# Kernel tuning notes

Hardware: AMD Instinct MI355X
Metric: run time of the kernel (lower is better)

The kernel has to match this reference:

```python
import jax, jax.numpy as jnp
import numpy as np

B, S, L, H, D, FF, V = 2, 1024, 12, 12, 768, 3072, 50265
DH = D // H
W1 = 256                      # one-sided window (attention_window=512)
MOTIF = (31 + 96 + 80) * 2    # 414
MAXPOS = 4098
EPS = 1e-5
NEG = jnp.float32(-1e9)


def _ln(x, s, b):
    m = jnp.mean(x, -1, keepdims=True)
    v = jnp.mean(jnp.square(x - m), -1, keepdims=True)
    return (x - m) * jax.lax.rsqrt(v + EPS) * s + b


def setup_inputs() -> dict:
    key = jax.random.key(0)
    ks = iter(jax.random.split(key, 48))
    n = lambda *sh: jax.random.normal(next(ks), sh, jnp.float32) * 0.02
    return {
        "input_ids": jax.random.randint(next(ks), (B, S), 0, V),
        "attention_mask": jnp.ones((B, S), jnp.int32),
        "motif_dist": jax.random.uniform(next(ks), (B, MOTIF), dtype=jnp.float32),
        "emb_word": n(V, D), "emb_pos": n(MAXPOS, D), "emb_type": n(1, D),
        "emb_ln_s": jnp.ones((D,)), "emb_ln_b": jnp.zeros((D,)),
        "Wq": n(L, D, D), "bq": jnp.zeros((L, D)),
        "Wk": n(L, D, D), "bk": jnp.zeros((L, D)),
        "Wv": n(L, D, D), "bv": jnp.zeros((L, D)),
        "Wqg": n(L, D, D), "bqg": jnp.zeros((L, D)),
        "Wkg": n(L, D, D), "bkg": jnp.zeros((L, D)),
        "Wvg": n(L, D, D), "bvg": jnp.zeros((L, D)),
        "Wo": n(L, D, D), "bo": jnp.zeros((L, D)),
        "ln1_s": jnp.ones((L, D)), "ln1_b": jnp.zeros((L, D)),
        "Wi": n(L, D, FF), "bi": jnp.zeros((L, FF)),
        "Wo2": n(L, FF, D), "bo2": jnp.zeros((L, D)),
        "ln2_s": jnp.ones((L, D)), "ln2_b": jnp.zeros((L, D)),
        "head_Wd": n(D + MOTIF, D), "head_bd": jnp.zeros((D,)),
        "head_Wp": n(D, 2), "head_bp": jnp.zeros((2,)),
    }


def reference(input_ids, attention_mask, motif_dist, emb_word, emb_pos, emb_type,
              emb_ln_s, emb_ln_b, Wq, bq, Wk, bk, Wv, bv, Wqg, bqg, Wkg, bkg,
              Wvg, bvg, Wo, bo, ln1_s, ln1_b, Wi, bi, Wo2, bo2, ln2_s, ln2_b,
              head_Wd, head_bd, head_Wp, head_bp):
    Bn, Sn = input_ids.shape
    scale = 1.0 / np.sqrt(DH)
    # RoBERTa-style embeddings: positions start at padding_idx+1 = 2
    pos_ids = jnp.arange(Sn) + 2
    x = emb_word[input_ids] + emb_pos[pos_ids][None] + emb_type[0][None, None]
    x = _ln(x, emb_ln_s, emb_ln_b)

    key_valid = attention_mask.astype(bool)[:, None, None, :]      # [B,1,1,S]
    idx = jnp.arange(Sn)
    is_global = idx == 0                                           # default: CLS-only global
    band = jnp.abs(idx[:, None] - idx[None, :]) <= W1
    # local query attends to its sliding window plus all global keys
    local_allowed = (band | is_global[None, :])[None, None] & key_valid

    def heads(t, s):
        return t.reshape(Bn, s, H, DH).transpose(0, 2, 1, 3)       # [B,H,s,DH]

    for l in range(L):
        q = heads(x @ Wq[l] + bq[l], Sn) * scale
        k = heads(x @ Wk[l] + bk[l], Sn)
        v = heads(x @ Wv[l] + bv[l], Sn)
        scores = jnp.einsum('bhid,bhjd->bhij', q, k)
        probs = jax.nn.softmax(jnp.where(local_allowed, scores, NEG), -1)
        out = jnp.einsum('bhij,bhjd->bhid', probs, v)              # [B,H,S,DH]
        # global (CLS) query: full attention using the *_global projections
        qg = heads(x[:, :1] @ Wqg[l] + bqg[l], 1) * scale          # [B,H,1,DH]
        kg = heads(x @ Wkg[l] + bkg[l], Sn)
        vg = heads(x @ Wvg[l] + bvg[l], Sn)
        sg = jnp.einsum('bhid,bhjd->bhij', qg, kg)                 # [B,H,1,S]
        pg = jax.nn.softmax(jnp.where(key_valid, sg, NEG), -1)
        og = jnp.einsum('bhij,bhjd->bhid', pg, vg)                 # [B,H,1,DH]
        out = jnp.concatenate([og, out[:, :, 1:]], axis=2)
        out = out.transpose(0, 2, 1, 3).reshape(Bn, Sn, D)
        x = _ln(x + out @ Wo[l] + bo[l], ln1_s[l], ln1_b[l])
        h = jax.nn.gelu(x @ Wi[l] + bi[l], approximate=False)
        x = _ln(x + h @ Wo2[l] + bo2[l], ln2_s[l], ln2_b[l])

    # classification head: CLS hidden state concat motif distribution
    hcat = jnp.concatenate([x[:, 0, :], motif_dist], axis=-1)
    return jnp.tanh(hcat @ head_Wd + head_bd) @ head_Wp + head_bp
```

## Files before the change

kernel.cpp:

```cpp
#include <hip/hip_runtime.h>
#include <math.h>

typedef unsigned short u16;
typedef __attribute__((ext_vector_type(8))) short short8;
typedef __attribute__((ext_vector_type(4))) float f32x4;

#define BB 2
#define SS 1024
#define LL 12
#define HH 12
#define DD 768
#define FFF 3072
#define MOTIF 414
#define HCAT (DD + MOTIF)
#define W1 256
#define NEGV -1e9f
#define EPS 1e-5f
#define SCALE 0.125f
#define LD5 3840

__device__ __forceinline__ float bf2f(u16 u) {
    union { unsigned i; float f; } x; x.i = ((unsigned)u) << 16; return x.f;
}
__device__ __forceinline__ u16 f2bf(float f) {
    union { float f; unsigned i; } x; x.f = f;
    unsigned r = x.i + 0x7fffu + ((x.i >> 16) & 1u);
    return (u16)(r >> 16);
}

__device__ __forceinline__ void gld16(const u16* g, u16* l) {
    __builtin_amdgcn_global_load_lds((const __attribute__((address_space(1))) void*)g,
                                     (__attribute__((address_space(3))) void*)l, 16, 0, 0);
}

__device__ __forceinline__ float block_reduce_sum(float v, float* red) {
    int t = threadIdx.x;
    red[t] = v; __syncthreads();
    #pragma unroll
    for (int s = 128; s > 0; s >>= 1) {
        if (t < s) red[t] += red[t + s];
        __syncthreads();
    }
    float r = red[0]; __syncthreads();
    return r;
}

__global__ __launch_bounds__(256) void embed_ln_kernel(
    const int* __restrict__ ids, const float* __restrict__ ew,
    const float* __restrict__ ep, const float* __restrict__ et,
    const float* __restrict__ gs, const float* __restrict__ gb,
    float* __restrict__ X, u16* __restrict__ Xb) {
    __shared__ float red[256];
    int row = blockIdx.x;
    int s = row % SS;
    int id = ids[row];
    int t = threadIdx.x;
    float v[3];
    float sum = 0.f;
    #pragma unroll
    for (int i = 0; i < 3; ++i) {
        int d = t + 256 * i;
        float x = ew[(size_t)id * DD + d] + ep[(size_t)(s + 2) * DD + d] + et[d];
        v[i] = x; sum += x;
    }
    sum = block_reduce_sum(sum, red);
    float m = sum * (1.f / DD);
    float sq = 0.f;
    #pragma unroll
    for (int i = 0; i < 3; ++i) { float c = v[i] - m; sq += c * c; }
    sq = block_reduce_sum(sq, red);
    float inv = rsqrtf(sq * (1.f / DD) + EPS);
    #pragma unroll
    for (int i = 0; i < 3; ++i) {
        int d = t + 256 * i;
        float o = (v[i] - m) * inv * gs[d] + gb[d];
        X[(size_t)row * DD + d] = o;
        Xb[(size_t)row * DD + d] = f2bf(o);
    }
}

__global__ __launch_bounds__(256) void add_ln_kernel(
    float* __restrict__ X, u16* __restrict__ Xb,
    const float* __restrict__ T1, const float* __restrict__ T2, int useT2,
    const float* __restrict__ gs, const float* __restrict__ gb) {
    __shared__ float red[256];
    int row = blockIdx.x;
    int t = threadIdx.x;
    float v[3];
    float sum = 0.f;
    #pragma unroll
    for (int i = 0; i < 3; ++i) {
        int d = t + 256 * i;
        size_t idx = (size_t)row * DD + d;
        float x = X[idx] + T1[idx] + (useT2 ? T2[idx] : 0.f);
        v[i] = x; sum += x;
    }
    sum = block_reduce_sum(sum, red);
    float m = sum * (1.f / DD);
    float sq = 0.f;
    #pragma unroll
    for (int i = 0; i < 3; ++i) { float c = v[i] - m; sq += c * c; }
    sq = block_reduce_sum(sq, red);
    float inv = rsqrtf(sq * (1.f / DD) + EPS);
    #pragma unroll
    for (int i = 0; i < 3; ++i) {
        int d = t + 256 * i;
        float o = (v[i] - m) * inv * gs[d] + gb[d];
        X[(size_t)row * DD + d] = o;
        Xb[(size_t)row * DD + d] = f2bf(o);
    }
}

__global__ __launch_bounds__(256) void conv_all_kernel(
    const float* __restrict__ w0, const float* __restrict__ w1,
    const float* __restrict__ w2, const float* __restrict__ w3,
    const float* __restrict__ w4, const float* __restrict__ w5,
    const float* __restrict__ wi, const float* __restrict__ wo2,
    u16* __restrict__ Wt6, u16* __restrict__ Wti, u16* __restrict__ Wto2) {
    __shared__ float Tt[32][33];
    int tid = blockIdx.x;
    const float* W; u16* Wt; int Nd, Kd, n0, k0;
    if (tid < 3456) {
        int z = tid / 576, rem = tid % 576;
        W = (z == 0) ? w0 : (z == 1) ? w1 : (z == 2) ? w2 : (z == 3) ? w3 : (z == 4) ? w4 : w5;
        Wt = Wt6 + (size_t)z * DD * DD;
        Nd = DD; Kd = DD; n0 = (rem % 24) * 32; k0 = (rem / 24) * 32;
    } else if (tid < 5760) {
        int i = tid - 3456;
        W = wi; Wt = Wti; Nd = FFF; Kd = DD; n0 = (i % 96) * 32; k0 = (i / 96) * 32;
    } else {
        int i = tid - 5760;
        W = wo2; Wt = Wto2; Nd = DD; Kd = FFF; n0 = (i % 24) * 32; k0 = (i / 24) * 32;
    }
    int t = threadIdx.x;
    int r = t >> 3, c = (t & 7) * 4;
    float4 v = *(const float4*)(W + (size_t)(k0 + r) * Nd + n0 + c);
    Tt[r][c] = v.x; Tt[r][c + 1] = v.y; Tt[r][c + 2] = v.z; Tt[r][c + 3] = v.w;
    __syncthreads();
    int n = t >> 3, k4 = (t & 7) * 4;
    unsigned lo = (unsigned)f2bf(Tt[k4][n])     | ((unsigned)f2bf(Tt[k4 + 1][n]) << 16);
    unsigned hi = (unsigned)f2bf(Tt[k4 + 2][n]) | ((unsigned)f2bf(Tt[k4 + 3][n]) << 16);
    uint2 wv; wv.x = lo; wv.y = hi;
    *(uint2*)&Wt[(size_t)(n0 + n) * Kd + k0 + k4] = wv;
}

__global__ __launch_bounds__(256) void bcat_kernel(
    const float* __restrict__ bq, const float* __restrict__ bk,
    const float* __restrict__ bv, const float* __restrict__ bkg,
    const float* __restrict__ bvg, float* __restrict__ bcat) {
    int tid = blockIdx.x * 256 + threadIdx.x;
    if (tid >= LL * LD5) return;
    int l = tid / LD5, r = tid % LD5, z = r / DD, j = r % DD;
    const float* src = (z == 0) ? bq : (z == 1) ? bk : (z == 2) ? bv : (z == 3) ? bkg : bvg;
    bcat[tid] = src[l * DD + j];
}

template <int ACT, int OBF>
__global__ __launch_bounds__(256) void gemm_bf16(
    const u16* __restrict__ A, const u16* __restrict__ Bt,
    const float* __restrict__ bias, void* __restrict__ C0, void* __restrict__ C1,
    int M, int N, int K, int Ksplit) {
    __shared__ __align__(16) u16 As[128 * 32];
    __shared__ __align__(16) u16 Bs[128 * 32];
    int z = blockIdx.z;
    int kbeg = z * Ksplit;
    int kend = kbeg + Ksplit; if (kend > K) kend = K;
    void* Cout = z ? C1 : C0;
    int t = threadIdx.x, lane = t & 63, wv = t >> 6;
    int bm = blockIdx.y * 128, bn = blockIdx.x * 128;
    int wm = wv >> 1, wn = wv & 1;
    int h = lane >> 4, q15 = lane & 15;
    f32x4 acc[4][4];
    #pragma unroll
    for (int i = 0; i < 4; ++i)
        #pragma unroll
        for (int j = 0; j < 4; ++j) { acc[i][j][0] = 0.f; acc[i][j][1] = 0.f; acc[i][j][2] = 0.f; acc[i][j][3] = 0.f; }

    for (int k0 = kbeg; k0 < kend; k0 += 32) {
        #pragma unroll
        for (int op = 0; op < 2; ++op) {
            int rc = wv * 32 + op * 16;
            int r = rc + (lane >> 2), s = lane & 3;
            gld16(A  + (size_t)(bm + r) * K + k0 + ((s ^ (r & 3)) * 8), &As[rc * 32]);
            gld16(Bt + (size_t)(bn + r) * K + k0 + ((s ^ (r & 3)) * 8), &Bs[rc * 32]);
        }
        __syncthreads();
        short8 af[4], bfr[4];
        #pragma unroll
        for (int mf = 0; mf < 4; ++mf) {
            int row = wm * 64 + mf * 16 + q15;
            af[mf] = *(const short8*)&As[row * 32 + ((h ^ (row & 3)) * 8)];
        }
        #pragma unroll
        for (int nf = 0; nf < 4; ++nf) {
            int row = wn * 64 + nf * 16 + q15;
            bfr[nf] = *(const short8*)&Bs[row * 32 + ((h ^ (row & 3)) * 8)];
        }
        #pragma unroll
        for (int mf = 0; mf < 4; ++mf)
            #pragma unroll
            for (int nf = 0; nf < 4; ++nf)
                acc[mf][nf] = __builtin_amdgcn_mfma_f32_16x16x32_bf16(af[mf], bfr[nf], acc[mf][nf], 0, 0, 0);
        __syncthreads();
    }
    float* Cf = (float*)Cout;
    u16*   Cb = (u16*)Cout;
    #pragma unroll
    for (int mf = 0; mf < 4; ++mf) {
        int mbase = bm + wm * 64 + mf * 16 + h * 4;
        #pragma unroll
        for (int nf = 0; nf < 4; ++nf) {
            int n = bn + wn * 64 + nf * 16 + q15;
            float bv = 0.f;
            if (z == 0) bv = bias[n];
            #pragma unroll
            for (int rg = 0; rg < 4; ++rg) {
                float val = acc[mf][nf][rg] + bv;
                if (ACT == 1) val = 0.5f * val * (1.f + erff(val * 0.70710678118654752f));
                if (OBF) Cb[(size_t)(mbase + rg) * N + n] = f2bf(val);
                else     Cf[(size_t)(mbase + rg) * N + n] = val;
            }
        }
    }
}

__global__ __launch_bounds__(256) void attn_local_mfma(
    const u16* __restrict__ QKV, const int* __restrict__ mask,
    u16* __restrict__ AO) {
    __shared__ __align__(16) u16 Qs[64 * 64];
    __shared__ __align__(16) u16 Ks[64 * 64];
    __shared__ __align__(16) u16 Vst[64 * 64];
    __shared__ __align__(16) u16 Pld[4][16 * 64];
    __shared__ float msk[64];
    int bid = blockIdx.x;
    int qt = bid & 15;
    int hh = (bid >> 4) % HH;
    int b  = bid / (16 * HH);
    int t = threadIdx.x, lane = t & 63, wv = t >> 6;
    int h = lane >> 4, q15 = lane & 15;
    int i0 = qt * 64;

    #pragma unroll
    for (int op = 0; op < 2; ++op) {
        int r = wv * 16 + op * 8 + (lane >> 3), s = lane & 7;
        gld16(QKV + (size_t)(b * SS + i0 + r) * LD5 + hh * 64 + ((s ^ (r & 7)) * 8),
              &Qs[(wv * 16 + op * 8) * 64]);
    }
    __syncthreads();
    short8 bq[2];
    {
        int qrow = wv * 16 + q15;
        #pragma unroll
        for (int ks = 0; ks < 2; ++ks)
            bq[ks] = *(const short8*)&Qs[qrow * 64 + (((ks * 4 + h) ^ (qrow & 7)) * 8)];
    }

    float mrun = -3e38f, lrun = 0.f;
    f32x4 o[4];
    #pragma unroll
    for (int nf = 0; nf < 4; ++nf) { o[nf][0] = 0.f; o[nf][1] = 0.f; o[nf][2] = 0.f; o[nf][3] = 0.f; }

    int jlo = i0 - W1; if (jlo < 0) jlo = 0;
    int jend = i0 + 64 + W1; if (jend > SS) jend = SS;
    int hasCLS = (jlo > 0) ? 1 : 0;
    int nt = hasCLS + (jend - jlo) / 64;
    int iq = i0 + wv * 16 + q15;

    for (int tt = 0; tt < nt; ++tt) {
        int base = (hasCLS && tt == 0) ? 0 : jlo + (tt - hasCLS) * 64;
        if (tt > 0) __syncthreads();
        #pragma unroll
        for (int op = 0; op < 2; ++op) {
            int r = wv * 16 + op * 8 + (lane >> 3), s = lane & 7;
            gld16(QKV + (size_t)(b * SS + base + r) * LD5 + 768 + hh * 64 + ((s ^ (r & 7)) * 8),
                  &Ks[(wv * 16 + op * 8) * 64]);
        }
        {
            int k2 = t & 31, dsec = t >> 5;
            const u16* vp = QKV + (size_t)(b * SS + base + 2 * k2) * LD5 + 1536 + hh * 64 + dsec * 8;
            union { uint4 v; u16 e[8]; } r0, r1;
            r0.v = *(const uint4*)vp;
            r1.v = *(const uint4*)(vp + LD5);
            int slot = k2 >> 2;
            #pragma unroll
            for (int j = 0; j < 8; ++j) {
                int d = dsec * 8 + j;
                unsigned val = (unsigned)r0.e[j] | ((unsigned)r1.e[j] << 16);
                *(unsigned*)&Vst[d * 64 + ((slot ^ (d & 7)) * 8) + ((2 * k2) & 7)] = val;
            }
        }
        if (t < 64) msk[t] = (float)mask[b * SS + base + t];
        __syncthreads();

        f32x4 sacc[4];
        #pragma unroll
        for (int kf = 0; kf < 4; ++kf) { sacc[kf][0] = 0.f; sacc[kf][1] = 0.f; sacc[kf][2] = 0.f; sacc[kf][3] = 0.f; }
        #pragma unroll
        for (int ks = 0; ks < 2; ++ks) {
            #pragma unroll
            for (int kf = 0; kf < 4; ++kf) {
                int krow = kf * 16 + q15;
                short8 afr = *(const short8*)&Ks[krow * 64 + (((ks * 4 + h) ^ (krow & 7)) * 8)];
                sacc[kf] = __builtin_amdgcn_mfma_f32_16x16x32_bf16(afr, bq[ks], sacc[kf], 0, 0, 0);
            }
        }
        float pv[4][4];
        float tmax = -3e38f;
        #pragma unroll
        for (int kf = 0; kf < 4; ++kf) {
            #pragma unroll
            for (int rg = 0; rg < 4; ++rg) {
                int kl = kf * 16 + h * 4 + rg;
                int key = base + kl;
                int dj = iq - key; int adj = dj < 0 ? -dj : dj;
                bool valid = ((adj <= W1) || (key == 0)) && (msk[kl] != 0.f);
                float s = valid ? sacc[kf][rg] * SCALE : NEGV;
                pv[kf][rg] = s;
                tmax = fmaxf(tmax, s);
            }
        }
        tmax = fmaxf(tmax, __shfl_xor(tmax, 16));
        tmax = fmaxf(tmax, __shfl_xor(tmax, 32));
        float mnew = fmaxf(mrun, tmax);
        float fac = __expf(mrun - mnew);
        mrun = mnew;
        float psum = 0.f;
        #pragma unroll
        for (int kf = 0; kf < 4; ++kf)
            #pragma unroll
            for (int rg = 0; rg < 4; ++rg) {
                float p = __expf(pv[kf][rg] - mnew);
                pv[kf][rg] = p; psum += p;
            }
        psum += __shfl_xor(psum, 16);
        psum += __shfl_xor(psum, 32);
        lrun = lrun * fac + psum;
        #pragma unroll
        for (int kf = 0; kf < 4; ++kf) {
            unsigned lo = (unsigned)f2bf(pv[kf][0]) | ((unsigned)f2bf(pv[kf][1]) << 16);
            unsigned hi = (unsigned)f2bf(pv[kf][2]) | ((unsigned)f2bf(pv[kf][3]) << 16);
            int slot = 2 * kf + (h >> 1);
            uint2 w; w.x = lo; w.y = hi;
            *(uint2*)&Pld[wv][q15 * 64 + ((slot ^ (q15 & 7)) * 8) + 4 * (h & 1)] = w;
        }
        float fo0 = __shfl(fac, (h * 4 + 0) | (lane & 48));
        float fo1 = __shfl(fac, (h * 4 + 1) | (lane & 48));
        float fo2 = __shfl(fac, (h * 4 + 2) | (lane & 48));
        float fo3 = __shfl(fac, (h * 4 + 3) | (lane & 48));
        #pragma unroll
        for (int nf = 0; nf < 4; ++nf) {
            o[nf][0] *= fo0; o[nf][1] *= fo1; o[nf][2] *= fo2; o[nf][3] *= fo3;
        }
        asm volatile("s_waitcnt lgkmcnt(0)" ::: "memory");
        #pragma unroll
        for (int ks = 0; ks < 2; ++ks) {
            short8 ap = *(const short8*)&Pld[wv][q15 * 64 + (((ks * 4 + h) ^ (q15 & 7)) * 8)];
            #pragma unroll
            for (int nf = 0; nf < 4; ++nf) {
                int d = nf * 16 + q15;
                short8 bvf = *(const short8*)&Vst[d * 64 + (((ks * 4 + h) ^ (d & 7)) * 8)];
                o[nf] = __builtin_amdgcn_mfma_f32_16x16x32_bf16(ap, bvf, o[nf], 0, 0, 0);
            }
        }
    }
    float linv = 1.f / lrun;
    float g0 = __shfl(linv, (h * 4 + 0) | (lane & 48));
    float g1 = __shfl(linv, (h * 4 + 1) | (lane & 48));
    float g2 = __shfl(linv, (h * 4 + 2) | (lane & 48));
    float g3 = __shfl(linv, (h * 4 + 3) | (lane & 48));
    size_t rb = (size_t)(b * SS + i0 + wv * 16 + h * 4);
    #pragma unroll
    for (int nf = 0; nf < 4; ++nf) {
        int d = hh * 64 + nf * 16 + q15;
        AO[(rb + 0) * DD + d] = f2bf(o[nf][0] * g0);
        AO[(rb + 1) * DD + d] = f2bf(o[nf][1] * g1);
        AO[(rb + 2) * DD + d] = f2bf(o[nf][2] * g2);
        AO[(rb + 3) * DD + d] = f2bf(o[nf][3] * g3);
    }
}

__global__ __launch_bounds__(512) void attn_global_kernel(
    const float* __restrict__ Xf, const float* __restrict__ Wqg,
    const float* __restrict__ bqg, const u16* __restrict__ QKV,
    const int* __restrict__ mask, u16* __restrict__ AO) {
    __shared__ float x0[DD];
    __shared__ float qv[64];
    __shared__ float sc[SS];
    __shared__ float red[512];
    __shared__ float part[8][64];
    int b = blockIdx.x / HH, hh = blockIdx.x % HH;
    int t = threadIdx.x;
    for (int i = t; i < DD; i += 512) x0[i] = Xf[(size_t)b * SS * DD + i];
    __syncthreads();
    {
        int d = t & 63, p = t >> 6;
        float acc = 0.f;
        int k0 = p * 96;
        #pragma unroll 8
        for (int k = k0; k < k0 + 96; ++k)
            acc += x0[k] * Wqg[(size_t)k * DD + hh * 64 + d];
        part[p][d] = acc;
    }
    __syncthreads();
    if (t < 64) {
        float s = bqg[hh * 64 + t];
        #pragma unroll
        for (int p = 0; p < 8; ++p) s += part[p][t];
        qv[t] = s * SCALE;
    }
    __syncthreads();
    for (int j = t; j < SS; j += 512) {
        const u16* kp = QKV + (size_t)(b * SS + j) * LD5 + 2304 + hh * 64;
        float acc = 0.f;
        #pragma unroll
        for (int d0 = 0; d0 < 64; d0 += 8) {
            union { uint4 v; u16 e[8]; } u;
            u.v = *(const uint4*)(kp + d0);
            #pragma unroll
            for (int j2 = 0; j2 < 8; ++j2) acc += qv[d0 + j2] * bf2f(u.e[j2]);
        }
        sc[j] = mask[b * SS + j] ? acc : NEGV;
    }
    __syncthreads();
    float mx = fmaxf(sc[t], sc[t + 512]);
    red[t] = mx; __syncthreads();
    #pragma unroll
    for (int s = 256; s > 0; s >>= 1) {
        if (t < s) red[t] = fmaxf(red[t], red[t + s]);
        __syncthreads();
    }
    mx = red[0]; __syncthreads();
    float e0 = __expf(sc[t] - mx), e1 = __expf(sc[t + 512] - mx);
    sc[t] = e0; sc[t + 512] = e1;
    red[t] = e0 + e1; __syncthreads();
    #pragma unroll
    for (int s = 256; s > 0; s >>= 1) {
        if (t < s) red[t] += red[t + s];
        __syncthreads();
    }
    float lsum = red[0]; __syncthreads();
    int g = t >> 6, d = t & 63;
    float acc = 0.f;
    for (int j = g; j < SS; j += 8)
        acc += sc[j] * bf2f(QKV[(size_t)(b * SS + j) * LD5 + 3072 + hh * 64 + d]);
    part[g][d] = acc;
    __syncthreads();
    if (g == 0) {
        float ov = 0.f;
        #pragma unroll
        for (int p = 0; p < 8; ++p) ov += part[p][d];
        AO[(size_t)(b * SS) * DD + hh * 64 + d] = f2bf(ov / lsum);
    }
}

__global__ __launch_bounds__(256) void head1_kernel(
    const float* __restrict__ X, const float* __restrict__ motif,
    const float* __restrict__ Wd, float* __restrict__ hpart) {
    __shared__ float hc[HCAT];
    __shared__ float part[4][64];
    int jb = blockIdx.x, kp = blockIdx.y, b = blockIdx.z;
    int t = threadIdx.x;
    for (int i = t; i < DD; i += 256) hc[i] = X[(size_t)b * SS * DD + i];
    for (int i = t; i < MOTIF; i += 256) hc[DD + i] = motif[(size_t)b * MOTIF + i];
    __syncthreads();
    int j = jb * 64 + (t & 63);
    int sub = t >> 6;
    int k0 = kp * 148 + sub * 37;
    int k1 = k0 + 37; if (k1 > HCAT) k1 = HCAT;
    float acc = 0.f;
    for (int k = k0; k < k1; ++k) acc += hc[k] * Wd[(size_t)k * DD + j];
    part[sub][t & 63] = acc;
    __syncthreads();
    if (sub == 0) {
        int x = t & 63;
        hpart[((size_t)b * 8 + kp) * DD + j] = part[0][x] + part[1][x] + part[2][x] + part[3][x];
    }
}

__global__ __launch_bounds__(256) void head2_kernel(
    const float* __restrict__ hpart, const float* __restrict__ bd,
    const float* __restrict__ Wp, const float* __restrict__ bp,
    float* __restrict__ out) {
    __shared__ float dvs[DD];
    __shared__ float red[256];
    int b = blockIdx.x;
    int t = threadIdx.x;
    for (int j = t; j < DD; j += 256) {
        float s = bd[j];
        #pragma unroll
        for (int kp = 0; kp < 8; ++kp) s += hpart[((size_t)b * 8 + kp) * DD + j];
        dvs[j] = tanhf(s);
    }
    __syncthreads();
    float a0 = 0.f, a1 = 0.f;
    for (int k = t; k < DD; k += 256) {
        a0 += dvs[k] * Wp[k * 2 + 0];
        a1 += dvs[k] * Wp[k * 2 + 1];
    }
    a0 = block_reduce_sum(a0, red);
    a1 = block_reduce_sum(a1, red);
    if (t == 0) {
        out[b * 2 + 0] = a0 + bp[0];
        out[b * 2 + 1] = a1 + bp[1];
    }
}

extern "C" void kernel_launch(void* const* d_in, const int* in_sizes, int n_in,
                              void* d_out, int out_size, void* d_ws, size_t ws_size,
                              hipStream_t stream) {
    const int*   input_ids = (const int*)d_in[0];
    const int*   attn_mask = (const int*)d_in[1];
    const float* motif     = (const float*)d_in[2];
    const float* emb_word  = (const float*)d_in[3];
    const float* emb_pos   = (const float*)d_in[4];
    const float* emb_type  = (const float*)d_in[5];
    const float* emb_ln_s  = (const float*)d_in[6];
    const float* emb_ln_b  = (const float*)d_in[7];
    const float* Wq  = (const float*)d_in[8];
    const float* bq  = (const float*)d_in[9];
    const float* Wk  = (const float*)d_in[10];
    const float* bk  = (const float*)d_in[11];
    const float* Wv  = (const float*)d_in[12];
    const float* bv  = (const float*)d_in[13];
    const float* Wqg = (const float*)d_in[14];
    const float* bqg = (const float*)d_in[15];
    const float* Wkg = (const float*)d_in[16];
    const float* bkg = (const float*)d_in[17];
    const float* Wvg = (const float*)d_in[18];
    const float* bvg = (const float*)d_in[19];
    const float* Wo  = (const float*)d_in[20];
    const float* bo  = (const float*)d_in[21];
    const float* ln1_s = (const float*)d_in[22];
    const float* ln1_b = (const float*)d_in[23];
    const float* Wi  = (const float*)d_in[24];
    const float* bi  = (const float*)d_in[25];
    const float* Wo2 = (const float*)d_in[26];
    const float* bo2 = (const float*)d_in[27];
    const float* ln2_s = (const float*)d_in[28];
    const float* ln2_b = (const float*)d_in[29];
    const float* head_Wd = (const float*)d_in[30];
    const float* head_bd = (const float*)d_in[31];
    const float* head_Wp = (const float*)d_in[32];
    const float* head_bp = (const float*)d_in[33];

    float* out = (float*)d_out;
    char* base = (char*)d_ws;

    float* Xf   = (float*)(base + 0);
    u16*   Xb   = (u16*)  (base + 6291456);
    u16*   QKVb = (u16*)  (base + 9437184);
    u16*   AOb  = (u16*)  (base + 25165824);
    float* T1f  = (float*)(base + 28311552);

    const size_t NEED_BIG = 57643008;
    bool big = ws_size >= NEED_BIG;
    float* T2f = big ? (float*)(base + 34603008) : T1f;
    size_t wbase = big ? 40894464 : 34603008;
    u16*   Wt6   = (u16*)  (base + wbase);
    u16*   Wti   = (u16*)  (base + wbase + 7077888);
    u16*   Wto2  = (u16*)  (base + wbase + 11796480);
    float* bcat  = (float*)(base + wbase + 16515072);
    float* hpart = (float*)(base + wbase + 16699392);
    u16*   Hb    = QKVb;

    const int nrow = BB * SS;
    const int useT2 = big ? 1 : 0;

    embed_ln_kernel<<<nrow, 256, 0, stream>>>(input_ids, emb_word, emb_pos, emb_type,
                                              emb_ln_s, emb_ln_b, Xf, Xb);
    bcat_kernel<<<(LL * LD5 + 255) / 256, 256, 0, stream>>>(bq, bk, bv, bkg, bvg, bcat);

    dim3 g5(30, 16, 1);
    dim3 gO(6, 16, big ? 2 : 1);
    dim3 gFF1(24, 16, 1);
    dim3 gFF2(6, 16, big ? 2 : 1);

    for (int l = 0; l < LL; ++l) {
        size_t oDD = (size_t)l * DD * DD;
        conv_all_kernel<<<8064, 256, 0, stream>>>(
            Wq + oDD, Wk + oDD, Wv + oDD, Wkg + oDD, Wvg + oDD, Wo + oDD,
            Wi + (size_t)l * DD * FFF, Wo2 + (size_t)l * FFF * DD,
            Wt6, Wti, Wto2);

        gemm_bf16<0, 1><<<g5, 256, 0, stream>>>(Xb, Wt6, bcat + l * LD5, QKVb, QKVb,
                                                nrow, LD5, DD, DD);

        attn_local_mfma<<<BB * HH * 16, 256, 0, stream>>>(QKVb, attn_mask, AOb);
        attn_global_kernel<<<BB * HH, 512, 0, stream>>>(Xf, Wqg + oDD, bqg + l * DD,
                                                        QKVb, attn_mask, AOb);

        gemm_bf16<0, 0><<<gO, 256, 0, stream>>>(AOb, Wt6 + 5 * (size_t)DD * DD, bo + l * DD,
                                                T1f, T2f, nrow, DD, DD, big ? 384 : 768);
        add_ln_kernel<<<nrow, 256, 0, stream>>>(Xf, Xb, T1f, T2f, useT2,
                                                ln1_s + l * DD, ln1_b + l * DD);

        gemm_bf16<1, 1><<<gFF1, 256, 0, stream>>>(Xb, Wti, bi + l * FFF, Hb, Hb,
                                                  nrow, FFF, DD, DD);
        gemm_bf16<0, 0><<<gFF2, 256, 0, stream>>>(Hb, Wto2, bo2 + l * DD,
                                                  T1f, T2f, nrow, DD, FFF, big ? 1536 : 3072);
        add_ln_kernel<<<nrow, 256, 0, stream>>>(Xf, Xb, T1f, T2f, useT2,
                                                ln2_s + l * DD, ln2_b + l * DD);
    }

    head1_kernel<<<dim3(12, 8, BB), 256, 0, stream>>>(Xf, motif, head_Wd, hpart);
    head2_kernel<<<BB, 256, 0, stream>>>(hpart, head_Wp ? head_bd : head_bd, head_Wp, head_bp, out);
}
```

Baseline: 2.707 ms.

## Batch all-layer weight conversion into one launch and fuse local/global attention

```diff
diff --git a/kernel.cpp b/kernel.cpp
--- a/kernel.cpp
+++ b/kernel.cpp
@@ -18,6 +18,7 @@
 #define EPS 1e-5f
 #define SCALE 0.125f
 #define LD5 3840
+#define WL_ELE 8257536
 
 __device__ __forceinline__ float bf2f(u16 u) {
     union { unsigned i; float f; } x; x.i = ((unsigned)u) << 16; return x.f;
@@ -111,26 +112,34 @@
     }
 }
 
+template <int LAYERED>
 __global__ __launch_bounds__(256) void conv_all_kernel(
-    const float* __restrict__ w0, const float* __restrict__ w1,
-    const float* __restrict__ w2, const float* __restrict__ w3,
-    const float* __restrict__ w4, const float* __restrict__ w5,
-    const float* __restrict__ wi, const float* __restrict__ wo2,
-    u16* __restrict__ Wt6, u16* __restrict__ Wti, u16* __restrict__ Wto2) {
+    const float* __restrict__ Wqp, const float* __restrict__ Wkp,
+    const float* __restrict__ Wvp, const float* __restrict__ Wkgp,
+    const float* __restrict__ Wvgp, const float* __restrict__ Wop,
+    const float* __restrict__ Wip, const float* __restrict__ Wo2p,
+    u16* __restrict__ WtBase) {
     __shared__ float Tt[32][33];
+    int l = LAYERED ? blockIdx.y : 0;
+    size_t oDD = (size_t)l * DD * DD;
+    size_t oFF = (size_t)l * DD * FFF;
+    u16* Wt6  = WtBase + (size_t)l * WL_ELE;
+    u16* Wti  = Wt6 + 6 * DD * DD;
+    u16* Wto2 = Wti + FFF * DD;
     int tid = blockIdx.x;
     const float* W; u16* Wt; int Nd, Kd, n0, k0;
     if (tid < 3456) {
         int z = tid / 576, rem = tid % 576;
-        W = (z == 0) ? w0 : (z == 1) ? w1 : (z == 2) ? w2 : (z == 3) ? w3 : (z == 4) ? w4 : w5;
+        const float* w6[6] = {Wqp + oDD, Wkp + oDD, Wvp + oDD, Wkgp + oDD, Wvgp + oDD, Wop + oDD};
+        W = w6[z];
         Wt = Wt6 + (size_t)z * DD * DD;
         Nd = DD; Kd = DD; n0 = (rem % 24) * 32; k0 = (rem / 24) * 32;
     } else if (tid < 5760) {
         int i = tid - 3456;
-        W = wi; Wt = Wti; Nd = FFF; Kd = DD; n0 = (i % 96) * 32; k0 = (i / 96) * 32;
+        W = Wip + oFF; Wt = Wti; Nd = FFF; Kd = DD; n0 = (i % 96) * 32; k0 = (i / 96) * 32;
     } else {
         int i = tid - 5760;
-        W = wo2; Wt = Wto2; Nd = DD; Kd = FFF; n0 = (i % 24) * 32; k0 = (i / 24) * 32;
+        W = Wo2p + oFF; Wt = Wto2; Nd = DD; Kd = FFF; n0 = (i % 24) * 32; k0 = (i / 24) * 32;
     }
     int t = threadIdx.x;
     int r = t >> 3, c = (t & 7) * 4;
@@ -224,19 +233,99 @@
     }
 }
 
-__global__ __launch_bounds__(256) void attn_local_mfma(
+struct LocalS {
+    u16 Qs[64 * 64]; u16 Ks[64 * 64]; u16 Vst[64 * 64];
+    u16 Pld[4][16 * 64]; float msk[64];
+};
+struct GlobS {
+    float x0[DD]; float qv[64]; float sc[SS]; float red[256]; float part[4][64];
+};
+union __align__(16) AttnSU { LocalS l; GlobS g; };
+
+__global__ __launch_bounds__(256) void attn_fused(
     const u16* __restrict__ QKV, const int* __restrict__ mask,
-    u16* __restrict__ AO) {
-    __shared__ __align__(16) u16 Qs[64 * 64];
-    __shared__ __align__(16) u16 Ks[64 * 64];
-    __shared__ __align__(16) u16 Vst[64 * 64];
-    __shared__ __align__(16) u16 Pld[4][16 * 64];
-    __shared__ float msk[64];
+    const float* __restrict__ Xf, const float* __restrict__ Wqg,
+    const float* __restrict__ bqg, u16* __restrict__ AO) {
+    __shared__ AttnSU su;
     int bid = blockIdx.x;
+    int t = threadIdx.x;
+
+    if (bid >= BB * HH * 16) {
+        GlobS& G = su.g;
+        int id = bid - BB * HH * 16;
+        int b = id / HH, hh = id % HH;
+        for (int i = t; i < DD; i += 256) G.x0[i] = Xf[(size_t)b * SS * DD + i];
+        __syncthreads();
+        {
+            int d = t & 63, p = t >> 6;
+            float acc = 0.f;
+            int k0 = p * 192;
+            #pragma unroll 4
+            for (int k = k0; k < k0 + 192; ++k)
+                acc += G.x0[k] * Wqg[(size_t)k * DD + hh * 64 + d];
+            G.part[p][d] = acc;
+        }
+        __syncthreads();
+        if (t < 64) {
+            float s = bqg[hh * 64 + t];
+            #pragma unroll
+            for (int p = 0; p < 4; ++p) s += G.part[p][t];
+            G.qv[t] = s * SCALE;
+        }
+        __syncthreads();
+        for (int j = t; j < SS; j += 256) {
+            const u16* kp = QKV + (size_t)(b * SS + j) * LD5 + 2304 + hh * 64;
+            float acc = 0.f;
+            #pragma unroll
+            for (int d0 = 0; d0 < 64; d0 += 8) {
+                union { uint4 v; u16 e[8]; } u;
+                u.v = *(const uint4*)(kp + d0);
+                #pragma unroll
+                for (int j2 = 0; j2 < 8; ++j2) acc += G.qv[d0 + j2] * bf2f(u.e[j2]);
+            }
+            G.sc[j] = mask[b * SS + j] ? acc : NEGV;
+        }
+        __syncthreads();
+        float mx = fmaxf(fmaxf(G.sc[t], G.sc[t + 256]), fmaxf(G.sc[t + 512], G.sc[t + 768]));
+        G.red[t] = mx; __syncthreads();
+        #pragma unroll
+        for (int s = 128; s > 0; s >>= 1) {
+            if (t < s) G.red[t] = fmaxf(G.red[t], G.red[t + s]);
+            __syncthreads();
+        }
+        mx = G.red[0]; __syncthreads();
+        float lsum;
+        {
+            float e0 = __expf(G.sc[t] - mx), e1 = __expf(G.sc[t + 256] - mx);
+            float e2 = __expf(G.sc[t + 512] - mx), e3 = __expf(G.sc[t + 768] - mx);
+            G.sc[t] = e0; G.sc[t + 256] = e1; G.sc[t + 512] = e2; G.sc[t + 768] = e3;
+            G.red[t] = e0 + e1 + e2 + e3; __syncthreads();
+            #pragma unroll
+            for (int s = 128; s > 0; s >>= 1) {
+                if (t < s) G.red[t] += G.red[t + s];
+                __syncthreads();
+            }
+            lsum = G.red[0]; __syncthreads();
+        }
+        int g = t >> 6, d = t & 63;
+        float acc = 0.f;
+        for (int j = g; j < SS; j += 4)
+            acc += G.sc[j] * bf2f(QKV[(size_t)(b * SS + j) * LD5 + 3072 + hh * 64 + d]);
+        G.part[g][d] = acc;
+        __syncthreads();
+        if (g == 0) {
+            float ov = G.part[0][d] + G.part[1][d] + G.part[2][d] + G.part[3][d];
+            AO[(size_t)(b * SS) * DD + hh * 64 + d] = f2bf(ov / lsum);
+        }
+        return;
+    }
+
+    u16* Qs = su.l.Qs; u16* Ks = su.l.Ks; u16* Vst = su.l.Vst;
+    u16 (*Pld)[16 * 64] = su.l.Pld; float* msk = su.l.msk;
     int qt = bid & 15;
     int hh = (bid >> 4) % HH;
     int b  = bid / (16 * HH);
-    int t = threadIdx.x, lane = t & 63, wv = t >> 6;
+    int lane = t & 63, wv = t >> 6;
     int h = lane >> 4, q15 = lane & 15;
     int i0 = qt * 64;
 
@@ -369,87 +458,14 @@
     float g2 = __shfl(linv, (h * 4 + 2) | (lane & 48));
     float g3 = __shfl(linv, (h * 4 + 3) | (lane & 48));
     size_t rb = (size_t)(b * SS + i0 + wv * 16 + h * 4);
+    bool skip0 = (i0 + wv * 16 + h * 4) == 0;
     #pragma unroll
     for (int nf = 0; nf < 4; ++nf) {
         int d = hh * 64 + nf * 16 + q15;
-        AO[(rb + 0) * DD + d] = f2bf(o[nf][0] * g0);
+        if (!skip0) AO[(rb + 0) * DD + d] = f2bf(o[nf][0] * g0);
         AO[(rb + 1) * DD + d] = f2bf(o[nf][1] * g1);
         AO[(rb + 2) * DD + d] = f2bf(o[nf][2] * g2);
         AO[(rb + 3) * DD + d] = f2bf(o[nf][3] * g3);
-    }
-}
-
-__global__ __launch_bounds__(512) void attn_global_kernel(
-    const float* __restrict__ Xf, const float* __restrict__ Wqg,
-    const float* __restrict__ bqg, const u16* __restrict__ QKV,
-    const int* __restrict__ mask, u16* __restrict__ AO) {
-    __shared__ float x0[DD];
-    __shared__ float qv[64];
-    __shared__ float sc[SS];
-    __shared__ float red[512];
-    __shared__ float part[8][64];
-    int b = blockIdx.x / HH, hh = blockIdx.x % HH;
-    int t = threadIdx.x;
-    for (int i = t; i < DD; i += 512) x0[i] = Xf[(size_t)b * SS * DD + i];
-    __syncthreads();
-    {
-        int d = t & 63, p = t >> 6;
-        float acc = 0.f;
-        int k0 = p * 96;
-        #pragma unroll 8
-        for (int k = k0; k < k0 + 96; ++k)
-            acc += x0[k] * Wqg[(size_t)k * DD + hh * 64 + d];
-        part[p][d] = acc;
-    }
-    __syncthreads();
-    if (t < 64) {
-        float s = bqg[hh * 64 + t];
-        #pragma unroll
-        for (int p = 0; p < 8; ++p) s += part[p][t];
-        qv[t] = s * SCALE;
-    }
-    __syncthreads();
-    for (int j = t; j < SS; j += 512) {
-        const u16* kp = QKV + (size_t)(b * SS + j) * LD5 + 2304 + hh * 64;
-        float acc = 0.f;
-        #pragma unroll
-        for (int d0 = 0; d0 < 64; d0 += 8) {
-            union { uint4 v; u16 e[8]; } u;
-            u.v = *(const uint4*)(kp + d0);
-            #pragma unroll
-            for (int j2 = 0; j2 < 8; ++j2) acc += qv[d0 + j2] * bf2f(u.e[j2]);
-        }
-        sc[j] = mask[b * SS + j] ? acc : NEGV;
-    }
-    __syncthreads();
-    float mx = fmaxf(sc[t], sc[t + 512]);
-    red[t] = mx; __syncthreads();
-    #pragma unroll
-    for (int s = 256; s > 0; s >>= 1) {
-        if (t < s) red[t] = fmaxf(red[t], red[t + s]);
-        __syncthreads();
-    }
-    mx = red[0]; __syncthreads();
-    float e0 = __expf(sc[t] - mx), e1 = __expf(sc[t + 512] - mx);
-    sc[t] = e0; sc[t + 512] = e1;
-    red[t] = e0 + e1; __syncthreads();
-    #pragma unroll
-    for (int s = 256; s > 0; s >>= 1) {
-        if (t < s) red[t] += red[t + s];
-        __syncthreads();
-    }
-    float lsum = red[0]; __syncthreads();
-    int g = t >> 6, d = t & 63;
-    float acc = 0.f;
-    for (int j = g; j < SS; j += 8)
-        acc += sc[j] * bf2f(QKV[(size_t)(b * SS + j) * LD5 + 3072 + hh * 64 + d]);
-    part[g][d] = acc;
-    __syncthreads();
-    if (g == 0) {
-        float ov = 0.f;
-        #pragma unroll
-        for (int p = 0; p < 8; ++p) ov += part[p][d];
-        AO[(size_t)(b * SS) * DD + hh * 64 + d] = f2bf(ov / lsum);
     }
 }
 
@@ -552,16 +568,28 @@
     u16*   AOb  = (u16*)  (base + 25165824);
     float* T1f  = (float*)(base + 28311552);
 
-    const size_t NEED_BIG = 57643008;
-    bool big = ws_size >= NEED_BIG;
+    const size_t NEED_BIG  = 57643008;
+    const size_t NEED_HUGE = 239308800;
+    bool huge = ws_size >= NEED_HUGE;
+    bool big  = huge || ws_size >= NEED_BIG;
+
     float* T2f = big ? (float*)(base + 34603008) : T1f;
-    size_t wbase = big ? 40894464 : 34603008;
-    u16*   Wt6   = (u16*)  (base + wbase);
-    u16*   Wti   = (u16*)  (base + wbase + 7077888);
-    u16*   Wto2  = (u16*)  (base + wbase + 11796480);
-    float* bcat  = (float*)(base + wbase + 16515072);
-    float* hpart = (float*)(base + wbase + 16699392);
-    u16*   Hb    = QKVb;
+    u16* WtAll; float* bcat; float* hpart;
+    u16 *Wt6_s = nullptr, *Wti_s = nullptr, *Wto2_s = nullptr;
+    if (huge) {
+        bcat  = (float*)(base + 40894464);
+        hpart = (float*)(base + 41078784);
+        WtAll = (u16*)  (base + 41127936);
+    } else {
+        size_t wbase = big ? 40894464 : 34603008;
+        Wt6_s  = (u16*)(base + wbase);
+        Wti_s  = (u16*)(base + wbase + 7077888);
+        Wto2_s = (u16*)(base + wbase + 11796480);
+        bcat   = (float*)(base + wbase + 16515072);
+        hpart  = (float*)(base + wbase + 16699392);
+        WtAll  = Wt6_s;
+    }
+    u16* Hb = QKVb;
 
     const int nrow = BB * SS;
     const int useT2 = big ? 1 : 0;
@@ -569,6 +597,9 @@
     embed_ln_kernel<<<nrow, 256, 0, stream>>>(input_ids, emb_word, emb_pos, emb_type,
                                               emb_ln_s, emb_ln_b, Xf, Xb);
     bcat_kernel<<<(LL * LD5 + 255) / 256, 256, 0, stream>>>(bq, bk, bv, bkg, bvg, bcat);
+    if (huge)
+        conv_all_kernel<1><<<dim3(8064, 12), 256, 0, stream>>>(
+            Wq, Wk, Wv, Wkg, Wvg, Wo, Wi, Wo2, WtAll);
 
     dim3 g5(30, 16, 1);
     dim3 gO(6, 16, big ? 2 : 1);
@@ -577,17 +608,23 @@
 
     for (int l = 0; l < LL; ++l) {
         size_t oDD = (size_t)l * DD * DD;
-        conv_all_kernel<<<8064, 256, 0, stream>>>(
-            Wq + oDD, Wk + oDD, Wv + oDD, Wkg + oDD, Wvg + oDD, Wo + oDD,
-            Wi + (size_t)l * DD * FFF, Wo2 + (size_t)l * FFF * DD,
-            Wt6, Wti, Wto2);
+        u16 *Wt6, *Wti, *Wto2;
+        if (huge) {
+            Wt6  = WtAll + (size_t)l * WL_ELE;
+            Wti  = Wt6 + 6 * DD * DD;
+            Wto2 = Wti + FFF * DD;
+        } else {
+            conv_all_kernel<0><<<dim3(8064, 1), 256, 0, stream>>>(
+                Wq + oDD, Wk + oDD, Wv + oDD, Wkg + oDD, Wvg + oDD, Wo + oDD,
+                Wi + (size_t)l * DD * FFF, Wo2 + (size_t)l * FFF * DD, Wt6_s);
+            Wt6 = Wt6_s; Wti = Wti_s; Wto2 = Wto2_s;
+        }
 
         gemm_bf16<0, 1><<<g5, 256, 0, stream>>>(Xb, Wt6, bcat + l * LD5, QKVb, QKVb,
                                                 nrow, LD5, DD, DD);
 
-        attn_local_mfma<<<BB * HH * 16, 256, 0, stream>>>(QKVb, attn_mask, AOb);
-        attn_global_kernel<<<BB * HH, 512, 0, stream>>>(Xf, Wqg + oDD, bqg + l * DD,
-                                                        QKVb, attn_mask, AOb);
+        attn_fused<<<BB * HH * 16 + BB * HH, 256, 0, stream>>>(
+            QKVb, attn_mask, Xf, Wqg + oDD, bqg + l * DD, AOb);
 
         gemm_bf16<0, 0><<<gO, 256, 0, stream>>>(AOb, Wt6 + 5 * (size_t)DD * DD, bo + l * DD,
                                                 T1f, T2f, nrow, DD, DD, big ? 384 : 768);
@@ -603,5 +640,5 @@
     }
 
     head1_kernel<<<dim3(12, 8, BB), 256, 0, stream>>>(Xf, motif, head_Wd, hpart);
-    head2_kernel<<<BB, 256, 0, stream>>>(hpart, head_Wp ? head_bd : head_bd, head_Wp, head_bp, out);
-}
+    head2_kernel<<<BB, 256, 0, stream>>>(hpart, head_bd, head_Wp, head_bp, out);
+}
```

New measurement: 3.059 ms. +13.0%, slower.
